# Kernel optimization log

Hardware: AMD Instinct MI355X
Metric: run time of the kernel (lower is better)

The kernel has to match this reference:

```python
import jax, jax.numpy as jnp
import numpy as np

B, C, H, W = 4, 256, 64, 64
CH = C // 2  # inner channels


def setup_inputs() -> dict:
    key = jax.random.key(0)
    ks = jax.random.split(key, 9)
    s_in = 1.0 / np.sqrt(C)
    s_w = 1.0 / np.sqrt(CH)
    return {
        "x": jax.random.normal(ks[0], (B, C, H, W), dtype=jnp.float32),
        "theta_w": jax.random.normal(ks[1], (CH, C), dtype=jnp.float32) * s_in,
        "theta_b": jax.random.normal(ks[2], (CH,), dtype=jnp.float32) * s_in,
        "phi_w": jax.random.normal(ks[3], (CH, C), dtype=jnp.float32) * s_in,
        "phi_b": jax.random.normal(ks[4], (CH,), dtype=jnp.float32) * s_in,
        "g_w": jax.random.normal(ks[5], (CH, C), dtype=jnp.float32) * s_in,
        "g_b": jax.random.normal(ks[6], (CH,), dtype=jnp.float32) * s_in,
        "W_w": jax.random.normal(ks[7], (C, CH), dtype=jnp.float32) * s_w,
        "W_b": jax.random.normal(ks[8], (C,), dtype=jnp.float32) * s_w,
    }


def _proj(x_flat, w, b):
    # 1x1 conv == channel matmul; x_flat: [B, C, N] -> [B, O, N]
    return jnp.einsum("oc,bcn->bon", w, x_flat) + b[None, :, None]


def reference(x, theta_w, theta_b, phi_w, phi_b, g_w, g_b, W_w, W_b):
    b, c, h, w = x.shape
    n = h * w
    xf = x.reshape(b, c, n)
    theta = _proj(xf, theta_w, theta_b)  # [B, CH, N]
    phi = _proj(xf, phi_w, phi_b)        # [B, CH, N]
    g = _proj(xf, g_w, g_b)              # [B, CH, N]
    # scores[b,i,j] = theta[:, :, i] . phi[:, :, j]; softmax over j
    attn = jax.nn.softmax(jnp.einsum("bci,bcj->bij", theta, phi), axis=-1)
    # torch: bmm(g_x, attn) -> out[b,c,i] = sum_j g[b,c,j] * attn[b,j,i]
    out = jnp.einsum("bcj,bji->bci", g, attn)  # [B, CH, N]
    out = jnp.einsum("oc,bcn->bon", W_w, out) + W_b[None, :, None]
    return out.reshape(b, c, h, w) + x
```

## Files before the change

### kernel.cpp

```cpp
#include <hip/hip_runtime.h>
#include <hip/hip_bf16.h>
#include <math.h>

#define BB    4
#define CC    256
#define CHN   128
#define NN    4096

typedef short short8 __attribute__((ext_vector_type(8)));
typedef float f32x4  __attribute__((ext_vector_type(4)));
typedef float f32x16 __attribute__((ext_vector_type(16)));
typedef unsigned short u16;
typedef u16  us4 __attribute__((ext_vector_type(4)));

#define MFMA16(a, b, c) __builtin_amdgcn_mfma_f32_16x16x32_bf16((a), (b), (c), 0, 0, 0)
#define MFMA32(a, b, c) __builtin_amdgcn_mfma_f32_32x32x16_bf16((a), (b), (c), 0, 0, 0)
#define LOG2E 1.4426950408889634f

#if __has_builtin(__builtin_amdgcn_exp2f)
#define EXP2F(x) __builtin_amdgcn_exp2f(x)
#else
#define EXP2F(x) exp2f(x)
#endif
#if __has_builtin(__builtin_amdgcn_logf)
#define LOG2F(x) __builtin_amdgcn_logf(x)
#else
#define LOG2F(x) log2f(x)
#endif

static __device__ __forceinline__ u16 f2bf(float f) {
    union { float f; unsigned u; } v; v.f = f;
    unsigned r = v.u + 0x7FFFu + ((v.u >> 16) & 1u);
    return (u16)(r >> 16);
}
static __device__ __forceinline__ unsigned pkbf(float a, float b) {
    __hip_bfloat162 h = __float22bfloat162_rn(make_float2(a, b));
    return *reinterpret_cast<unsigned*>(&h);
}
static __device__ __forceinline__ int sw128(int row, int u) {
    return row * 128 + ((u ^ (row & 7)) << 3);
}

__global__ __launch_bounds__(256) void k_cvtw(
    const float* __restrict__ tw, const float* __restrict__ pw,
    const float* __restrict__ gw, const float* __restrict__ Ww,
    u16* __restrict__ wall)
{
    int idx = (blockIdx.x * 256 + threadIdx.x) * 4;
    const float* s = (idx < 32768) ? tw
                   : (idx < 65536) ? pw
                   : (idx < 98304) ? gw : Ww;
    float sc = (idx < 32768) ? LOG2E : 1.0f;
    float4 v = *(const float4*)(s + (idx & 32767));
    us4 r = { f2bf(v.x * sc), f2bf(v.y * sc), f2bf(v.z * sc), f2bf(v.w * sc) };
    *(us4*)(wall + idx) = r;
}

__global__ __launch_bounds__(512) void k_proj(
    const float* __restrict__ x, const u16* __restrict__ wall,
    const float* __restrict__ tb, const float* __restrict__ pb,
    const float* __restrict__ gbias,
    u16* __restrict__ tht, u16* __restrict__ pht, u16* __restrict__ gg)
{
    __shared__ u16 xs[64 * 264];
    __shared__ u16 gbuf[128 * 68];
    const int tid = threadIdx.x;
    const int n0  = blockIdx.x * 64;
    const int b   = blockIdx.y;
    const int ln  = tid & 15, q = (tid >> 4) & 3, wid = tid >> 6;
    const int ow  = wid & 1, nw = wid >> 1;

    for (int p = 0; p < 8; ++p) {
        int id = p * 512 + tid;
        int c = id >> 4, n4 = (id & 15) * 4;
        float4 xv = *(const float4*)(x + ((size_t)b * CC + c) * NN + n0 + n4);
        xs[(n4 + 0) * 264 + c] = f2bf(xv.x);
        xs[(n4 + 1) * 264 + c] = f2bf(xv.y);
        xs[(n4 + 2) * 264 + c] = f2bf(xv.z);
        xs[(n4 + 3) * 264 + c] = f2bf(xv.w);
    }
    __syncthreads();

    short8 bfr[8];
    #pragma unroll
    for (int ks = 0; ks < 8; ++ks)
        bfr[ks] = *(const short8*)(&xs[(nw * 16 + ln) * 264 + ks * 32 + q * 8]);

    for (int pr = 0; pr < 3; ++pr) {
        const u16* wsrc = wall + pr * 32768;
        f32x4 acc[4];
        #pragma unroll
        for (int oo = 0; oo < 4; ++oo) acc[oo] = (f32x4){0.f, 0.f, 0.f, 0.f};
        for (int ks = 0; ks < 8; ++ks) {
            short8 a[4];
            #pragma unroll
            for (int oo = 0; oo < 4; ++oo)
                a[oo] = *(const short8*)(wsrc + (size_t)(ow*64 + oo*16 + ln) * 256 + ks*32 + q*8);
            #pragma unroll
            for (int oo = 0; oo < 4; ++oo)
                acc[oo] = MFMA16(a[oo], bfr[ks], acc[oo]);
        }
        const float* bias = (pr == 0) ? tb : (pr == 1 ? pb : gbias);
        const float bsc = (pr == 0) ? LOG2E : 1.0f;
        if (pr < 2) {
            u16* dst = (pr == 0) ? tht : pht;
            const int n = n0 + nw * 16 + ln;
            #pragma unroll
            for (int oo = 0; oo < 4; ++oo) {
                int o = ow * 64 + oo * 16 + q * 4;
                float4 bv = *(const float4*)(bias + o);
                f32x4 v = acc[oo];
                uint2 r = { pkbf(v.x + bv.x * bsc, v.y + bv.y * bsc),
                            pkbf(v.z + bv.z * bsc, v.w + bv.w * bsc) };
                *(uint2*)(dst + ((size_t)b * NN + n) * CHN + o) = r;
            }
        } else {
            const int nl = nw * 16 + ln;
            #pragma unroll
            for (int oo = 0; oo < 4; ++oo) {
                int o = ow * 64 + oo * 16 + q * 4;
                float4 bv = *(const float4*)(bias + o);
                f32x4 v = acc[oo];
                gbuf[(o + 0) * 68 + nl] = f2bf(v.x + bv.x);
                gbuf[(o + 1) * 68 + nl] = f2bf(v.y + bv.y);
                gbuf[(o + 2) * 68 + nl] = f2bf(v.z + bv.z);
                gbuf[(o + 3) * 68 + nl] = f2bf(v.w + bv.w);
            }
            __syncthreads();
            for (int p = 0; p < 4; ++p) {
                int id = p * 512 + tid;
                int c = id >> 4, n4 = (id & 15) * 4;
                us4 r = *(const us4*)(&gbuf[c * 68 + n4]);
                *(us4*)(gg + ((size_t)b * CHN + c) * NN + n0 + n4) = r;
            }
        }
    }
}

__global__ __launch_bounds__(512, 2) void k_rowsum(
    const u16* __restrict__ tht, const u16* __restrict__ pht,
    float* __restrict__ Z)
{
    __shared__ u16 ph_s[2][128 * 128];
    const int tid = threadIdx.x;
    const int j0  = blockIdx.x * 256;
    const int i00 = blockIdx.y * 1024;
    const int b   = blockIdx.z;
    const int l   = tid & 63, w = tid >> 6;
    const int lm  = l & 31, lh = l >> 5;
    const u16* thb = tht + (size_t)b * NN * CHN;
    const u16* phb = pht + (size_t)b * NN * CHN;

    short8 ar[8];
    #pragma unroll
    for (int ks = 0; ks < 8; ++ks)
        ar[ks] = *(const short8*)(thb + (size_t)(j0 + w*32 + lm) * CHN + ks*16 + lh*8);

    for (int p = 0; p < 4; ++p) {
        int id = p * 512 + tid;
        int row = id >> 4, u = id & 15;
        short8 v = *(const short8*)(phb + (size_t)(i00 + row) * CHN + u * 8);
        *(short8*)(&ph_s[0][sw128(row, u)]) = v;
    }

    float zp[16];
    #pragma unroll
    for (int r = 0; r < 16; ++r) zp[r] = 0.f;

    for (int is = 0; is < 8; ++is) {
        __syncthreads();
        if (is < 7) {
            for (int p = 0; p < 4; ++p) {
                int id = p * 512 + tid;
                int row = id >> 4, u = id & 15;
                short8 v = *(const short8*)(phb + (size_t)(i00 + (is+1)*128 + row) * CHN + u * 8);
                *(short8*)(&ph_s[(is + 1) & 1][sw128(row, u)]) = v;
            }
        }
        const u16* cur = ph_s[is & 1];

        #pragma unroll
        for (int ii = 0; ii < 4; ++ii) {
            f32x16 s;
            #pragma unroll
            for (int r = 0; r < 16; ++r) s[r] = 0.f;
            #pragma unroll
            for (int ks = 0; ks < 8; ++ks) {
                short8 bfrag = *(const short8*)(&cur[sw128(ii*32 + lm, ks*2 + lh)]);
                s = MFMA32(ar[ks], bfrag, s);
            }
            #pragma unroll
            for (int r = 0; r < 16; ++r) zp[r] += EXP2F(s[r]);
        }
    }

    float zr[16];
    #pragma unroll
    for (int r = 0; r < 16; ++r) {
        float v = zp[r];
        v += __shfl_xor(v, 1);
        v += __shfl_xor(v, 2);
        v += __shfl_xor(v, 4);
        v += __shfl_xor(v, 8);
        v += __shfl_xor(v, 16);
        zr[r] = v;
    }
    if (lm == 0) {
        #pragma unroll
        for (int r = 0; r < 16; ++r) {
            int j = j0 + w*32 + (r & 3) + 8*(r >> 2) + 4*lh;
            atomicAdd(&Z[(size_t)b * NN + j], zr[r]);
        }
    }
}

__global__ __launch_bounds__(512, 2) void k_attn(
    const u16* __restrict__ tht, const u16* __restrict__ pht,
    const u16* __restrict__ gg, const float* __restrict__ Z,
    u16* __restrict__ innerT)
{
    __shared__ u16 th_s[128 * 128];
    __shared__ u16 g_s [128 * 128];
    __shared__ u16 E_s [256 * 128];
    const int tid = threadIdx.x;
    const int i0  = blockIdx.x * 256;
    const int jq  = blockIdx.y;
    const int b   = blockIdx.z;
    const int l   = tid & 63, w = tid >> 6;
    const int lm  = l & 31, lh = l >> 5;
    const int h1  = w & 1;
    const int h2  = w >> 1;

    const u16*  thb = tht + (size_t)b * NN * CHN;
    const u16*  ggb = gg  + (size_t)b * CHN * NN;
    const float* Zb = Z   + (size_t)b * NN;

    int srow[4], su[4];
    #pragma unroll
    for (int p = 0; p < 4; ++p) {
        int id = p * 512 + tid;
        srow[p] = id >> 4; su[p] = id & 15;
    }

    short8 phr[2][8];
    #pragma unroll
    for (int ii = 0; ii < 2; ++ii)
        #pragma unroll
        for (int ks = 0; ks < 8; ++ks)
            phr[ii][ks] = *(const short8*)(pht + ((size_t)b * NN + i0 + h2*64 + ii*32 + lm) * CHN + ks*16 + lh*8);

    #pragma unroll
    for (int p = 0; p < 4; ++p) {
        short8 tv = *(const short8*)(thb + (size_t)(jq*1024 + srow[p]) * CHN + su[p] * 8);
        short8 gv = *(const short8*)(ggb + (size_t)srow[p] * NN + jq*1024 + su[p] * 8);
        *(short8*)(&th_s[sw128(srow[p], su[p])]) = tv;
        *(short8*)(&g_s [sw128(srow[p], su[p])]) = gv;
    }
    __syncthreads();

    f32x16 pacc[2][2];
    #pragma unroll
    for (int cc = 0; cc < 2; ++cc)
        #pragma unroll
        for (int ii = 0; ii < 2; ++ii)
            #pragma unroll
            for (int r = 0; r < 16; ++r) pacc[cc][ii][r] = 0.f;

    for (int s = 0; s < 8; ++s) {
        const int j0 = jq * 1024 + s * 128;

        short8 thn[4], gn[4];
        if (s < 7) {
            const int jn = j0 + 128;
            #pragma unroll
            for (int p = 0; p < 4; ++p) {
                thn[p] = *(const short8*)(thb + (size_t)(jn + srow[p]) * CHN + su[p] * 8);
                gn[p]  = *(const short8*)(ggb + (size_t)srow[p] * NN + jn + su[p] * 8);
            }
        }

        #pragma unroll
        for (int jj = 0; jj < 2; ++jj) {
            const int jbase = h1*64 + jj*32;
            f32x16 cinit;
            #pragma unroll
            for (int rq = 0; rq < 4; ++rq) {
                float4 Lv = *(const float4*)(Zb + j0 + jbase + rq*8 + lh*4);
                cinit[rq*4 + 0] = -LOG2F(Lv.x);
                cinit[rq*4 + 1] = -LOG2F(Lv.y);
                cinit[rq*4 + 2] = -LOG2F(Lv.z);
                cinit[rq*4 + 3] = -LOG2F(Lv.w);
            }
            f32x16 s0 = cinit, s1 = cinit;
            #pragma unroll
            for (int ks = 0; ks < 8; ++ks) {
                short8 a = *(const short8*)(&th_s[sw128(jbase + lm, ks*2 + lh)]);
                s0 = MFMA32(a, phr[0][ks], s0);
                s1 = MFMA32(a, phr[1][ks], s1);
            }
            #pragma unroll
            for (int ii = 0; ii < 2; ++ii) {
                const f32x16 sv = ii ? s1 : s0;
                const int ri = h2*64 + ii*32 + lm;
                #pragma unroll
                for (int rq = 0; rq < 4; ++rq) {
                    const int jl = jbase + rq*8 + lh*4;
                    uint2 e = { pkbf(EXP2F(sv[rq*4+0]), EXP2F(sv[rq*4+1])),
                                pkbf(EXP2F(sv[rq*4+2]), EXP2F(sv[rq*4+3])) };
                    *(uint2*)(&E_s[ri*128 + (((jl >> 3) ^ (ri & 7)) << 3) + (jl & 7)]) = e;
                }
            }
        }
        __syncthreads();

        if (s < 7) {
            #pragma unroll
            for (int p = 0; p < 4; ++p)
                *(short8*)(&th_s[sw128(srow[p], su[p])]) = thn[p];
        }

        #pragma unroll
        for (int ks = 0; ks < 8; ++ks) {
            short8 eb[2];
            #pragma unroll
            for (int ii = 0; ii < 2; ++ii)
                eb[ii] = *(const short8*)(&E_s[sw128(h2*64 + ii*32 + lm, ks*2 + lh)]);
            #pragma unroll
            for (int cc = 0; cc < 2; ++cc) {
                short8 ag = *(const short8*)(&g_s[sw128(h1*64 + cc*32 + lm, ks*2 + lh)]);
                pacc[cc][0] = MFMA32(ag, eb[0], pacc[cc][0]);
                pacc[cc][1] = MFMA32(ag, eb[1], pacc[cc][1]);
            }
        }
        __syncthreads();

        if (s < 7) {
            #pragma unroll
            for (int p = 0; p < 4; ++p)
                *(short8*)(&g_s[sw128(srow[p], su[p])]) = gn[p];
        }
    }

    u16* dst = innerT + ((size_t)jq * BB + b) * (size_t)NN * CHN;
    #pragma unroll
    for (int cc = 0; cc < 2; ++cc)
        #pragma unroll
        for (int ii = 0; ii < 2; ++ii) {
            const int i = i0 + h2*64 + ii*32 + lm;
            const f32x16 v = pacc[cc][ii];
            #pragma unroll
            for (int rq = 0; rq < 4; ++rq) {
                const int c0 = h1*64 + cc*32 + rq*8 + lh*4;
                uint2 r = { pkbf(v[rq*4+0], v[rq*4+1]),
                            pkbf(v[rq*4+2], v[rq*4+3]) };
                *(uint2*)(dst + (size_t)i * CHN + c0) = r;
            }
        }
}

__global__ __launch_bounds__(512, 2) void k_final(
    const u16* __restrict__ innerT, const float* __restrict__ x,
    const u16* __restrict__ Wwbf, const float* __restrict__ Wb,
    float* __restrict__ out)
{
    __shared__ u16 w_s[256 * 128];
    __shared__ u16 a_s[64 * 128];
    const int tid = threadIdx.x;
    const int n0  = blockIdx.x * 64;
    const int b   = blockIdx.y;
    const int l   = tid & 63, w = tid >> 6;
    const int lm  = l & 31, lh = l >> 5;

    for (int p = 0; p < 8; ++p) {
        int id = p * 512 + tid;
        int row = id >> 4, u = id & 15;
        *(short8*)(&w_s[sw128(row, u)]) = *(const short8*)(Wwbf + (size_t)row * CHN + u * 8);
    }
    __syncthreads();

    short8 aw[8];
    #pragma unroll
    for (int ks = 0; ks < 8; ++ks)
        aw[ks] = *(const short8*)(&w_s[sw128(w*32 + lm, ks*2 + lh)]);

    f32x16 acc[2];
    #pragma unroll
    for (int nt = 0; nt < 2; ++nt)
        #pragma unroll
        for (int r = 0; r < 16; ++r) acc[nt][r] = 0.f;

    for (int jq = 0; jq < 4; ++jq) {
        __syncthreads();
        for (int p = 0; p < 2; ++p) {
            int id = p * 512 + tid;
            int row = id >> 4, u = id & 15;
            *(short8*)(&a_s[sw128(row, u)]) =
                *(const short8*)(innerT + (((size_t)jq * BB + b) * NN + n0 + row) * CHN + u * 8);
        }
        __syncthreads();
        #pragma unroll
        for (int ks = 0; ks < 8; ++ks) {
            short8 bn[2];
            #pragma unroll
            for (int nt = 0; nt < 2; ++nt)
                bn[nt] = *(const short8*)(&a_s[sw128(nt*32 + lm, ks*2 + lh)]);
            acc[0] = MFMA32(aw[ks], bn[0], acc[0]);
            acc[1] = MFMA32(aw[ks], bn[1], acc[1]);
        }
    }

    #pragma unroll
    for (int nt = 0; nt < 2; ++nt) {
        const int n = n0 + nt*32 + lm;
        #pragma unroll
        for (int r = 0; r < 16; ++r) {
            const int o = w*32 + (r & 3) + 8*(r >> 2) + 4*lh;
            const size_t idx = ((size_t)b * CC + o) * NN + n;
            out[idx] = acc[nt][r] + Wb[o] + x[idx];
        }
    }
}

extern "C" void kernel_launch(void* const* d_in, const int* in_sizes, int n_in,
                              void* d_out, int out_size, void* d_ws, size_t ws_size,
                              hipStream_t stream)
{
    const float* x  = (const float*)d_in[0];
    const float* tw = (const float*)d_in[1];
    const float* tb = (const float*)d_in[2];
    const float* pw = (const float*)d_in[3];
    const float* pb = (const float*)d_in[4];
    const float* gw = (const float*)d_in[5];
    const float* gb = (const float*)d_in[6];
    const float* Ww = (const float*)d_in[7];
    const float* Wb = (const float*)d_in[8];
    float* out = (float*)d_out;

    char* p = (char*)d_ws;
    const size_t proj_u16 = (size_t)BB * NN * CHN;
    u16*   tht    = (u16*)p;   p += proj_u16 * 2;
    u16*   pht    = (u16*)p;   p += proj_u16 * 2;
    u16*   gg     = (u16*)p;   p += proj_u16 * 2;
    u16*   wall   = (u16*)p;   p += (size_t)131072 * 2;
    float* Z      = (float*)p; p += (size_t)BB * NN * 4;
    u16*   innerT = (u16*)p;

    hipMemsetAsync(Z, 0, (size_t)BB * NN * sizeof(float), stream);
    k_cvtw  <<<128, 256, 0, stream>>>(tw, pw, gw, Ww, wall);
    k_proj  <<<dim3(64, BB), 512, 0, stream>>>(x, wall, tb, pb, gb, tht, pht, gg);
    k_rowsum<<<dim3(16, 4, BB), 512, 0, stream>>>(tht, pht, Z);
    k_attn  <<<dim3(16, 4, BB), 512, 0, stream>>>(tht, pht, gg, Z, innerT);
    k_final <<<dim3(64, BB), 512, 0, stream>>>(innerT, x, wall + 98304, Wb, out);
}
```

Before: 196.4 us.

## Keep attention probabilities in registers and double-buffer theta/g tiles in k_attn

Restructures k_attn so each wave owns 32 query rows and all 128 channels. The exp'd score tile is repacked with cross-half-wave shuffles directly into MFMA B-operand registers, which removes the E_s shared-memory round trip and one barrier per step. Theta and g tiles are double-buffered in LDS so the next tile is written while the current one is consumed. The -log2 of the row sums is precomputed once by a new small k_log kernel instead of being recomputed per block. The cost is an extra kernel launch and the same LDS footprint, now spent on the double buffers.

```diff
diff --git a/kernel.cpp b/kernel.cpp
--- a/kernel.cpp
+++ b/kernel.cpp
@@ -214,26 +214,32 @@
     }
 }
 
+__global__ __launch_bounds__(256) void k_log(
+    const float* __restrict__ Z, float* __restrict__ L)
+{
+    int idx = (blockIdx.x * 256 + threadIdx.x) * 4;
+    float4 z = *(const float4*)(Z + idx);
+    float4 r = { -LOG2F(z.x), -LOG2F(z.y), -LOG2F(z.z), -LOG2F(z.w) };
+    *(float4*)(L + idx) = r;
+}
+
 __global__ __launch_bounds__(512, 2) void k_attn(
     const u16* __restrict__ tht, const u16* __restrict__ pht,
-    const u16* __restrict__ gg, const float* __restrict__ Z,
+    const u16* __restrict__ gg, const float* __restrict__ Lbuf,
     u16* __restrict__ innerT)
 {
-    __shared__ u16 th_s[128 * 128];
-    __shared__ u16 g_s [128 * 128];
-    __shared__ u16 E_s [256 * 128];
+    __shared__ u16 th_s[2][128 * 128];
+    __shared__ u16 g_s [2][128 * 128];
     const int tid = threadIdx.x;
     const int i0  = blockIdx.x * 256;
     const int jq  = blockIdx.y;
     const int b   = blockIdx.z;
-    const int l   = tid & 63, w = tid >> 6;
-    const int lm  = l & 31, lh = l >> 5;
-    const int h1  = w & 1;
-    const int h2  = w >> 1;
+    const int w   = tid >> 6;
+    const int lm  = tid & 31, lh = (tid >> 5) & 1;
 
     const u16*  thb = tht + (size_t)b * NN * CHN;
     const u16*  ggb = gg  + (size_t)b * CHN * NN;
-    const float* Zb = Z   + (size_t)b * NN;
+    const float* Lb = Lbuf + (size_t)b * NN;
 
     int srow[4], su[4];
     #pragma unroll
@@ -242,120 +248,104 @@
         srow[p] = id >> 4; su[p] = id & 15;
     }
 
-    short8 phr[2][8];
-    #pragma unroll
-    for (int ii = 0; ii < 2; ++ii)
-        #pragma unroll
-        for (int ks = 0; ks < 8; ++ks)
-            phr[ii][ks] = *(const short8*)(pht + ((size_t)b * NN + i0 + h2*64 + ii*32 + lm) * CHN + ks*16 + lh*8);
+    short8 phr[8];
+    #pragma unroll
+    for (int ks = 0; ks < 8; ++ks)
+        phr[ks] = *(const short8*)(pht + ((size_t)b * NN + i0 + w*32 + lm) * CHN + ks*16 + lh*8);
 
     #pragma unroll
     for (int p = 0; p < 4; ++p) {
         short8 tv = *(const short8*)(thb + (size_t)(jq*1024 + srow[p]) * CHN + su[p] * 8);
         short8 gv = *(const short8*)(ggb + (size_t)srow[p] * NN + jq*1024 + su[p] * 8);
-        *(short8*)(&th_s[sw128(srow[p], su[p])]) = tv;
-        *(short8*)(&g_s [sw128(srow[p], su[p])]) = gv;
+        *(short8*)(&th_s[0][sw128(srow[p], su[p])]) = tv;
+        *(short8*)(&g_s [0][sw128(srow[p], su[p])]) = gv;
     }
     __syncthreads();
 
-    f32x16 pacc[2][2];
-    #pragma unroll
-    for (int cc = 0; cc < 2; ++cc)
-        #pragma unroll
-        for (int ii = 0; ii < 2; ++ii)
-            #pragma unroll
-            for (int r = 0; r < 16; ++r) pacc[cc][ii][r] = 0.f;
+    f32x16 pacc[4];
+    #pragma unroll
+    for (int ct = 0; ct < 4; ++ct)
+        #pragma unroll
+        for (int r = 0; r < 16; ++r) pacc[ct][r] = 0.f;
 
     for (int s = 0; s < 8; ++s) {
-        const int j0 = jq * 1024 + s * 128;
+        const int j0s = jq * 1024 + s * 128;
+        const u16* thc = th_s[s & 1];
+        const u16* gc  = g_s [s & 1];
 
         short8 thn[4], gn[4];
         if (s < 7) {
-            const int jn = j0 + 128;
             #pragma unroll
             for (int p = 0; p < 4; ++p) {
-                thn[p] = *(const short8*)(thb + (size_t)(jn + srow[p]) * CHN + su[p] * 8);
-                gn[p]  = *(const short8*)(ggb + (size_t)srow[p] * NN + jn + su[p] * 8);
-            }
-        }
-
-        #pragma unroll
-        for (int jj = 0; jj < 2; ++jj) {
-            const int jbase = h1*64 + jj*32;
-            f32x16 cinit;
+                thn[p] = *(const short8*)(thb + (size_t)(j0s + 128 + srow[p]) * CHN + su[p] * 8);
+                gn[p]  = *(const short8*)(ggb + (size_t)srow[p] * NN + j0s + 128 + su[p] * 8);
+            }
+        }
+
+        #pragma unroll
+        for (int jj = 0; jj < 4; ++jj) {
+            f32x16 sv;
             #pragma unroll
             for (int rq = 0; rq < 4; ++rq) {
-                float4 Lv = *(const float4*)(Zb + j0 + jbase + rq*8 + lh*4);
-                cinit[rq*4 + 0] = -LOG2F(Lv.x);
-                cinit[rq*4 + 1] = -LOG2F(Lv.y);
-                cinit[rq*4 + 2] = -LOG2F(Lv.z);
-                cinit[rq*4 + 3] = -LOG2F(Lv.w);
-            }
-            f32x16 s0 = cinit, s1 = cinit;
+                float4 Lv = *(const float4*)(Lb + j0s + jj*32 + rq*8 + lh*4);
+                sv[rq*4 + 0] = Lv.x; sv[rq*4 + 1] = Lv.y;
+                sv[rq*4 + 2] = Lv.z; sv[rq*4 + 3] = Lv.w;
+            }
             #pragma unroll
             for (int ks = 0; ks < 8; ++ks) {
-                short8 a = *(const short8*)(&th_s[sw128(jbase + lm, ks*2 + lh)]);
-                s0 = MFMA32(a, phr[0][ks], s0);
-                s1 = MFMA32(a, phr[1][ks], s1);
-            }
-            #pragma unroll
-            for (int ii = 0; ii < 2; ++ii) {
-                const f32x16 sv = ii ? s1 : s0;
-                const int ri = h2*64 + ii*32 + lm;
+                short8 a = *(const short8*)(&thc[sw128(jj*32 + lm, ks*2 + lh)]);
+                sv = MFMA32(a, phr[ks], sv);
+            }
+            unsigned e0 = pkbf(EXP2F(sv[0]),  EXP2F(sv[1]));
+            unsigned e1 = pkbf(EXP2F(sv[2]),  EXP2F(sv[3]));
+            unsigned e2 = pkbf(EXP2F(sv[4]),  EXP2F(sv[5]));
+            unsigned e3 = pkbf(EXP2F(sv[6]),  EXP2F(sv[7]));
+            unsigned e4 = pkbf(EXP2F(sv[8]),  EXP2F(sv[9]));
+            unsigned e5 = pkbf(EXP2F(sv[10]), EXP2F(sv[11]));
+            unsigned e6 = pkbf(EXP2F(sv[12]), EXP2F(sv[13]));
+            unsigned e7 = pkbf(EXP2F(sv[14]), EXP2F(sv[15]));
+            unsigned s0 = __shfl_xor(e0, 32), s1 = __shfl_xor(e1, 32);
+            unsigned s2 = __shfl_xor(e2, 32), s3 = __shfl_xor(e3, 32);
+            unsigned s4 = __shfl_xor(e4, 32), s5 = __shfl_xor(e5, 32);
+            unsigned s6 = __shfl_xor(e6, 32), s7 = __shfl_xor(e7, 32);
+            union { unsigned u[4]; short8 v; } f[2];
+            f[0].u[0] = lh ? s2 : e0;  f[0].u[1] = lh ? s3 : e1;
+            f[0].u[2] = lh ? e2 : s0;  f[0].u[3] = lh ? e3 : s1;
+            f[1].u[0] = lh ? s6 : e4;  f[1].u[1] = lh ? s7 : e5;
+            f[1].u[2] = lh ? e6 : s4;  f[1].u[3] = lh ? e7 : s5;
+            #pragma unroll
+            for (int h = 0; h < 2; ++h) {
                 #pragma unroll
-                for (int rq = 0; rq < 4; ++rq) {
-                    const int jl = jbase + rq*8 + lh*4;
-                    uint2 e = { pkbf(EXP2F(sv[rq*4+0]), EXP2F(sv[rq*4+1])),
-                                pkbf(EXP2F(sv[rq*4+2]), EXP2F(sv[rq*4+3])) };
-                    *(uint2*)(&E_s[ri*128 + (((jl >> 3) ^ (ri & 7)) << 3) + (jl & 7)]) = e;
+                for (int ct = 0; ct < 4; ++ct) {
+                    short8 ag = *(const short8*)(&gc[sw128(ct*32 + lm, jj*4 + h*2 + lh)]);
+                    pacc[ct] = MFMA32(ag, f[h].v, pacc[ct]);
                 }
             }
         }
+
+        if (s < 7) {
+            const int nb = (s + 1) & 1;
+            #pragma unroll
+            for (int p = 0; p < 4; ++p) {
+                *(short8*)(&th_s[nb][sw128(srow[p], su[p])]) = thn[p];
+                *(short8*)(&g_s [nb][sw128(srow[p], su[p])]) = gn[p];
+            }
+        }
         __syncthreads();
-
-        if (s < 7) {
-            #pragma unroll
-            for (int p = 0; p < 4; ++p)
-                *(short8*)(&th_s[sw128(srow[p], su[p])]) = thn[p];
-        }
-
-        #pragma unroll
-        for (int ks = 0; ks < 8; ++ks) {
-            short8 eb[2];
-            #pragma unroll
-            for (int ii = 0; ii < 2; ++ii)
-                eb[ii] = *(const short8*)(&E_s[sw128(h2*64 + ii*32 + lm, ks*2 + lh)]);
-            #pragma unroll
-            for (int cc = 0; cc < 2; ++cc) {
-                short8 ag = *(const short8*)(&g_s[sw128(h1*64 + cc*32 + lm, ks*2 + lh)]);
-                pacc[cc][0] = MFMA32(ag, eb[0], pacc[cc][0]);
-                pacc[cc][1] = MFMA32(ag, eb[1], pacc[cc][1]);
-            }
-        }
-        __syncthreads();
-
-        if (s < 7) {
-            #pragma unroll
-            for (int p = 0; p < 4; ++p)
-                *(short8*)(&g_s[sw128(srow[p], su[p])]) = gn[p];
-        }
     }
 
     u16* dst = innerT + ((size_t)jq * BB + b) * (size_t)NN * CHN;
-    #pragma unroll
-    for (int cc = 0; cc < 2; ++cc)
-        #pragma unroll
-        for (int ii = 0; ii < 2; ++ii) {
-            const int i = i0 + h2*64 + ii*32 + lm;
-            const f32x16 v = pacc[cc][ii];
-            #pragma unroll
-            for (int rq = 0; rq < 4; ++rq) {
-                const int c0 = h1*64 + cc*32 + rq*8 + lh*4;
-                uint2 r = { pkbf(v[rq*4+0], v[rq*4+1]),
-                            pkbf(v[rq*4+2], v[rq*4+3]) };
-                *(uint2*)(dst + (size_t)i * CHN + c0) = r;
-            }
-        }
+    const int i = i0 + w*32 + lm;
+    #pragma unroll
+    for (int ct = 0; ct < 4; ++ct) {
+        #pragma unroll
+        for (int rq = 0; rq < 4; ++rq) {
+            const int c0 = ct*32 + rq*8 + lh*4;
+            uint2 r = { pkbf(pacc[ct][rq*4+0], pacc[ct][rq*4+1]),
+                        pkbf(pacc[ct][rq*4+2], pacc[ct][rq*4+3]) };
+            *(uint2*)(dst + (size_t)i * CHN + c0) = r;
+        }
+    }
 }
 
 __global__ __launch_bounds__(512, 2) void k_final(
@@ -443,12 +433,14 @@
     u16*   gg     = (u16*)p;   p += proj_u16 * 2;
     u16*   wall   = (u16*)p;   p += (size_t)131072 * 2;
     float* Z      = (float*)p; p += (size_t)BB * NN * 4;
+    float* Lbuf   = (float*)p; p += (size_t)BB * NN * 4;
     u16*   innerT = (u16*)p;
 
     hipMemsetAsync(Z, 0, (size_t)BB * NN * sizeof(float), stream);
     k_cvtw  <<<128, 256, 0, stream>>>(tw, pw, gw, Ww, wall);
     k_proj  <<<dim3(64, BB), 512, 0, stream>>>(x, wall, tb, pb, gb, tht, pht, gg);
     k_rowsum<<<dim3(16, 4, BB), 512, 0, stream>>>(tht, pht, Z);
-    k_attn  <<<dim3(16, 4, BB), 512, 0, stream>>>(tht, pht, gg, Z, innerT);
+    k_log   <<<16, 256, 0, stream>>>(Z, Lbuf);
+    k_attn  <<<dim3(16, 4, BB), 512, 0, stream>>>(tht, pht, gg, Lbuf, innerT);
     k_final <<<dim3(64, BB), 512, 0, stream>>>(innerT, x, wall + 98304, Wb, out);
 }
```

Result: faster. 191.8 us (-2.4%).
